# Optimization experiments

Hardware: AMD Instinct MI355X
Metric: run time of the kernel (lower is better)

## Reference

```python
import jax, jax.numpy as jnp
import numpy as np

C = 1.0          # Poincare ball curvature
EPS = 1e-7
MAX_TANH_ARG = 1.0 - 1e-5
K = 5            # topk neighbors (hardcoded in the module)


def _norm(x):
    return jnp.clip(jnp.linalg.norm(x, axis=-1, keepdims=True), EPS)


def expmap0(u):
    # exp map at origin: tanh(sqrt(c)||u||) * u / (sqrt(c)||u||)
    sc = jnp.sqrt(C)
    n = _norm(u)
    return jnp.tanh(sc * n) * u / (sc * n)


def logmap0(x):
    # log map at origin: artanh(sqrt(c)||x||) * x / (sqrt(c)||x||)
    sc = jnp.sqrt(C)
    n = _norm(x)
    arg = jnp.clip(sc * n, EPS, MAX_TANH_ARG)
    return jnp.arctanh(arg) * x / (sc * n)


def mobius_add(x, y):
    x2 = jnp.sum(x * x, axis=-1, keepdims=True)
    y2 = jnp.sum(y * y, axis=-1, keepdims=True)
    xy = jnp.sum(x * y, axis=-1, keepdims=True)
    num = (1.0 + 2.0 * C * xy + C * y2) * x + (1.0 - C * x2) * y
    den = 1.0 + 2.0 * C * xy + (C * C) * x2 * y2
    return num / (den + EPS)


def setup_inputs() -> dict:
    key = jax.random.key(0)
    k1, k2, k3, k4 = jax.random.split(key, 4)
    B, SEQ_DIM, HYP_DIM, N = 2048, 768, 128, 100000
    z_seq = jax.random.normal(k1, (B, SEQ_DIM), dtype=jnp.float32)
    # node embeddings must lie inside the unit ball; scale keeps norms ~0.57
    node_emb = 0.05 * jax.random.normal(k2, (N, HYP_DIM), dtype=jnp.float32)
    W = 0.02 * jax.random.normal(k3, (HYP_DIM, SEQ_DIM), dtype=jnp.float32)
    b = jnp.zeros((HYP_DIM,), dtype=jnp.float32)
    return {"z_seq": z_seq, "node_emb": node_emb, "W": W, "b": b}


def reference(z_seq, node_emb, W, b):
    # linear projection (dropout is identity in eval mode)
    z_proj = z_seq @ W.T + b                     # (B, D)
    z_hyp = expmap0(z_proj)                      # (B, D) in Poincare ball
    # no-grad nearest-node lookup in tangent space
    z_tan = logmap0(z_hyp)                       # (B, D)
    n_tan = logmap0(node_emb)                    # (N, D)
    # squared euclidean distances (monotone in cdist -> same topk indices)
    d2 = (jnp.sum(z_tan * z_tan, axis=-1, keepdims=True)
          - 2.0 * (z_tan @ n_tan.T)
          + jnp.sum(n_tan * n_tan, axis=-1)[None, :])  # (B, N)
    _, idx = jax.lax.top_k(-d2, K)               # (B, K) smallest distances
    near = jnp.mean(node_emb[idx], axis=1)       # (B, D) gather-mean
    z_fused = mobius_add(z_hyp, near)
    return (z_fused, z_hyp)
```

## Files before the change

kernel.cpp:

```cpp
#include <hip/hip_runtime.h>
#include <hip/hip_bf16.h>
#include <math.h>

#define EPSF 1e-7f
#define MAXT 0.99999f

typedef __attribute__((ext_vector_type(8))) short short8v;
typedef __attribute__((ext_vector_type(4))) float f32x4;

constexpr int Bb = 2048;
constexpr int Ss = 768;
constexpr int Dd = 128;
constexpr int Nn = 100000;
constexpr int Kk = 5;
constexpr int HALF = Bb * Dd;
constexpr int NT = 128;
constexpr int TILE_BYTES = NT * Dd * 2;
constexpr float SBIAS = 16.0f;

constexpr int NCH8 = 8;
constexpr int CH8 = Nn / NCH8;
constexpr int TIL8 = 98;
constexpr int PAD8 = TIL8 * NT;
constexpr int RQ = 64;

constexpr int NCH16 = 16;
constexpr int CH16 = Nn / NCH16;
constexpr int TIL16 = (CH16 + NT - 1) / NT;
constexpr int RT = 128;

static __device__ __forceinline__ ushort f2bf(float x) {
  __hip_bfloat16 h = __float2bfloat16(x);
  return *reinterpret_cast<ushort*>(&h);
}

static __device__ __forceinline__ float med3f(float a, float b, float c) {
  float r;
  asm("v_med3_f32 %0, %1, %2, %3" : "=v"(r) : "v"(a), "v"(b), "v"(c));
  return r;
}

static __device__ __forceinline__ void ins5f(float* k, float v) {
  const float n0 = fminf(k[0], v);
  const float n1 = med3f(k[0], k[1], v);
  const float n2 = med3f(k[1], k[2], v);
  const float n3 = med3f(k[2], k[3], v);
  const float n4 = med3f(k[3], k[4], v);
  k[0] = n0; k[1] = n1; k[2] = n2; k[3] = n3; k[4] = n4;
}

#define INS5(TV, TI, V, ID) do { \
  const float _v = (V); const int _id = (ID); \
  if (_v < TV[4]) { \
    TV[4] = _v; TI[4] = _id; \
    if (TV[4] < TV[3]) { float _t=TV[3];TV[3]=TV[4];TV[4]=_t;int _u=TI[3];TI[3]=TI[4];TI[4]=_u; } \
    if (TV[3] < TV[2]) { float _t=TV[2];TV[2]=TV[3];TV[3]=_t;int _u=TI[2];TI[2]=TI[3];TI[3]=_u; } \
    if (TV[2] < TV[1]) { float _t=TV[1];TV[1]=TV[2];TV[2]=_t;int _u=TI[1];TI[1]=TI[2];TI[2]=_u; } \
    if (TV[1] < TV[0]) { float _t=TV[0];TV[0]=TV[1];TV[1]=_t;int _u=TI[0];TI[0]=TI[1];TI[1]=_u; } \
  } } while(0)

#define LXLT(V,I,V2,I2) ((V) < (V2) || ((V) == (V2) && (I) < (I2)))
#define INS5L(TV, TI, V, ID) do { \
  const float _v = (V); const int _id = (ID); \
  if (LXLT(_v,_id,TV[4],TI[4])) { \
    TV[4]=_v; TI[4]=_id; \
    if (LXLT(TV[4],TI[4],TV[3],TI[3])) { float _t=TV[3];TV[3]=TV[4];TV[4]=_t;int _u=TI[3];TI[3]=TI[4];TI[4]=_u; } \
    if (LXLT(TV[3],TI[3],TV[2],TI[2])) { float _t=TV[2];TV[2]=TV[3];TV[3]=_t;int _u=TI[2];TI[2]=TI[3];TI[3]=_u; } \
    if (LXLT(TV[2],TI[2],TV[1],TI[1])) { float _t=TV[1];TV[1]=TV[2];TV[2]=_t;int _u=TI[1];TI[1]=TI[2];TI[2]=_u; } \
    if (LXLT(TV[1],TI[1],TV[0],TI[0])) { float _t=TV[0];TV[0]=TV[1];TV[1]=_t;int _u=TI[0];TI[0]=TI[1];TI[1]=_u; } \
  } } while(0)

static __device__ __forceinline__ void proj_body(
    const float* __restrict__ zseq, const float* __restrict__ W,
    const float* __restrict__ bias, float* __restrict__ outH,
    ushort* __restrict__ ztb, int blk,
    float (*zrow)[768], float (*zp)[128], float (*php)[128], float* rno)
{
  const int tid = threadIdx.x;
  const int d = tid & 127, h = tid >> 7;
  const int r0 = blk * 8;

  {
    const float4* src = reinterpret_cast<const float4*>(zseq + (size_t)r0 * Ss);
    float4* dst = reinterpret_cast<float4*>(&zrow[0][0]);
    #pragma unroll
    for (int i = 0; i < 6; ++i) dst[i * 256 + tid] = src[i * 256 + tid];
  }
  __syncthreads();

  float acc[8];
  #pragma unroll
  for (int r = 0; r < 8; ++r) acc[r] = 0.f;
  const float4* w4 = reinterpret_cast<const float4*>(W + (size_t)d * Ss) + h * 96;
  for (int j = 0; j < 96; ++j) {
    const float4 w = w4[j];
    const int kb = h * 384 + j * 4;
    #pragma unroll
    for (int r = 0; r < 8; ++r) {
      const float4 z = *reinterpret_cast<const float4*>(&zrow[r][kb]);
      acc[r] = fmaf(z.x, w.x, acc[r]);
      acc[r] = fmaf(z.y, w.y, acc[r]);
      acc[r] = fmaf(z.z, w.z, acc[r]);
      acc[r] = fmaf(z.w, w.w, acc[r]);
    }
  }
  #pragma unroll
  for (int r = 0; r < 8; ++r) {
    if (h == 0) zp[r][d] = acc[r]; else php[r][d] = acc[r];
  }
  __syncthreads();
  if (tid < 128) {
    const float bv = bias[d];
    #pragma unroll
    for (int r = 0; r < 8; ++r) zp[r][d] = zp[r][d] + php[r][d] + bv;
  }
  __syncthreads();

  const int wv = tid >> 6, ln = tid & 63;
  if (tid < 128) {
    #pragma unroll
    for (int rr = 0; rr < 4; ++rr) {
      const int r = wv * 4 + rr;
      float v = zp[r][ln] * zp[r][ln] + zp[r][ln + 64] * zp[r][ln + 64];
      #pragma unroll
      for (int off = 32; off > 0; off >>= 1) v += __shfl_xor(v, off);
      if (ln == 0) rno[r] = v;
    }
  }
  __syncthreads();
  if (tid < 128) {
    #pragma unroll
    for (int r = 0; r < 8; ++r) {
      const float n = fmaxf(sqrtf(rno[r]), EPSF);
      const float zh = tanhf(n) * zp[r][d] / n;
      outH[(size_t)(r0 + r) * Dd + d] = zh;
      zp[r][d] = zh;
    }
  }
  __syncthreads();
  if (tid < 128) {
    #pragma unroll
    for (int rr = 0; rr < 4; ++rr) {
      const int r = wv * 4 + rr;
      float v = zp[r][ln] * zp[r][ln] + zp[r][ln + 64] * zp[r][ln + 64];
      #pragma unroll
      for (int off = 32; off > 0; off >>= 1) v += __shfl_xor(v, off);
      if (ln == 0) rno[r] = v;
    }
  }
  __syncthreads();
  if (tid < 128) {
    #pragma unroll
    for (int r = 0; r < 8; ++r) {
      const float m = fmaxf(sqrtf(rno[r]), EPSF);
      const float a = atanhf(fminf(m, MAXT));
      ztb[(size_t)(r0 + r) * Dd + d] = f2bf(a * zp[r][d] / m);
    }
  }
}

__global__ __launch_bounds__(256) void k_proj(
    const float* __restrict__ zseq, const float* __restrict__ W,
    const float* __restrict__ bias, float* __restrict__ outH,
    ushort* __restrict__ ztb)
{
  __shared__ __align__(16) float zrow[8][768];
  __shared__ float zp[8][128];
  __shared__ float php[8][128];
  __shared__ float rno[8];
  proj_body(zseq, W, bias, outH, ztb, blockIdx.x, zrow, zp, php, rno);
}

__global__ __launch_bounds__(256) void k_prep(
    const float* __restrict__ zseq, const float* __restrict__ W,
    const float* __restrict__ bias, float* __restrict__ outH,
    ushort* __restrict__ ztb, const float* __restrict__ emb,
    ushort* __restrict__ embsw, float* __restrict__ cpad)
{
  __shared__ __align__(16) float zrow[8][768];
  __shared__ float zp[8][128];
  __shared__ float php[8][128];
  __shared__ float rno[8];

  if (blockIdx.x < Bb / 8) {
    proj_body(zseq, W, bias, outH, ztb, blockIdx.x, zrow, zp, php, rno);
    return;
  }

  const int wv = threadIdx.x >> 6, ln = threadIdx.x & 63;
  const int p = (blockIdx.x - Bb / 8) * 4 + wv;
  const int chunk = p / PAD8;
  const int local = p - chunk * PAD8;
  const bool real = local < CH8;
  const int node = chunk * CH8 + local;
  float2 v = make_float2(0.f, 0.f);
  if (real) v = *reinterpret_cast<const float2*>(emb + (size_t)node * Dd + ln * 2);
  float t = v.x * v.x + v.y * v.y;
  #pragma unroll
  for (int off = 32; off > 0; off >>= 1) t += __shfl_xor(t, off);

  const float E = fmaxf(sqrtf(t), EPSF);
  const float a = atanhf(fminf(E, MAXT));
  const float s = a / E;
  const float m2s = -2.f * s;

  const int tt = local >> 7, nd = local & 127;
  ushort2 w; w.x = f2bf(m2s * v.x); w.y = f2bf(m2s * v.y);
  char* dst = reinterpret_cast<char*>(embsw)
            + ((size_t)((chunk * TIL8 + tt) * NT + nd) << 8)
            + ((ln * 4) ^ ((nd & 7) << 4));
  *reinterpret_cast<ushort2*>(dst) = w;

  if (ln == 0) cpad[p] = real ? (s * s * t + SBIAS) : 3.0e38f;
}

__global__ __launch_bounds__(1024, 4) void k_topk8(
    const ushort* __restrict__ ztb, const ushort* __restrict__ embsw,
    const float* __restrict__ cpad, float* __restrict__ candV,
    int* __restrict__ candI)
{
  __shared__ __align__(16) ushort Bsm[2][NT * Dd];
  __shared__ __align__(16) float cb[2][NT];

  const int tid = threadIdx.x;
  const int ln = tid & 63;
  const int wv8 = (tid >> 6) & 7;
  const int qh = tid >> 9;
  const int ln15 = ln & 15;
  const int g = ln >> 4;
  const int chunk = blockIdx.x & 7;
  const int rowBase = (blockIdx.x >> 3) * RQ;
  const int qBase = rowBase + qh * 32;
  const char* embc = reinterpret_cast<const char*>(embsw)
                   + (size_t)chunk * (TIL8 * TILE_BYTES);
  const float* cch = cpad + (size_t)chunk * PAD8;

  short8v zfr[2][4];
  #pragma unroll
  for (int f = 0; f < 2; ++f)
    #pragma unroll
    for (int ks = 0; ks < 4; ++ks)
      zfr[f][ks] = *reinterpret_cast<const short8v*>(
          ztb + (size_t)(qBase + 16 * f + ln15) * Dd + 32 * ks + 8 * g);

  int rdoff[4];
  #pragma unroll
  for (int ks = 0; ks < 4; ++ks)
    rdoff[ks] = (wv8 * 16 + ln15) * 256 + ((ks * 64 + g * 16) ^ ((ln15 & 7) << 4));
  const int coff = wv8 * 64 + g * 16;
  const unsigned lanebase = (unsigned)(wv8 * 16 + 4 * g);

  float tv0[5], tv1[5];
  const float KINIT = __uint_as_float(0x7F7FFFFFu);
  #pragma unroll
  for (int q = 0; q < 5; ++q) { tv0[q] = KINIT; tv1[q] = KINIT; }

  const char* srcP = embc + tid * 16;
  const float* cbP = cch + tid;

  auto stage = [&](int buf) {
    char* lb = reinterpret_cast<char*>(&Bsm[buf][0]) + tid * 16;
    #pragma unroll
    for (int i = 0; i < 2; ++i) {
      __builtin_amdgcn_global_load_lds(
          (const __attribute__((address_space(1))) unsigned int*)(srcP + i * 16384),
          (__attribute__((address_space(3))) unsigned int*)(lb + i * 16384),
          16, 0, 0);
    }
    if (tid < NT) {
      __builtin_amdgcn_global_load_lds(
          (const __attribute__((address_space(1))) unsigned int*)cbP,
          (__attribute__((address_space(3))) unsigned int*)(&cb[buf][tid]),
          4, 0, 0);
    }
    srcP += TILE_BYTES;
    cbP += NT;
  };

  asm volatile("s_waitcnt vmcnt(0)" ::: "memory");
  stage(0);
  stage(1);

  for (int t = 0; t < TIL8; ++t) {
    const int buf = t & 1;
    if (t == TIL8 - 1) {
      asm volatile("s_waitcnt vmcnt(0)" ::: "memory");
    } else if (tid < 128) {
      asm volatile("s_waitcnt vmcnt(3)" ::: "memory");
    } else {
      asm volatile("s_waitcnt vmcnt(2)" ::: "memory");
    }
    __builtin_amdgcn_s_barrier();

    const char* bbase = reinterpret_cast<const char*>(&Bsm[buf][0]);
    short8v ae[4];
    #pragma unroll
    for (int ks = 0; ks < 4; ++ks)
      ae[ks] = *reinterpret_cast<const short8v*>(bbase + rdoff[ks]);
    const f32x4 cinit = *reinterpret_cast<const f32x4*>(
        reinterpret_cast<const char*>(&cb[buf][0]) + coff);

    __builtin_amdgcn_s_setprio(1);
    f32x4 a0 = __builtin_amdgcn_mfma_f32_16x16x32_bf16(ae[0], zfr[0][0], cinit, 0, 0, 0);
    f32x4 a1 = __builtin_amdgcn_mfma_f32_16x16x32_bf16(ae[0], zfr[1][0], cinit, 0, 0, 0);
    #pragma unroll
    for (int ks = 1; ks < 4; ++ks) {
      a0 = __builtin_amdgcn_mfma_f32_16x16x32_bf16(ae[ks], zfr[0][ks], a0, 0, 0, 0);
      a1 = __builtin_amdgcn_mfma_f32_16x16x32_bf16(ae[ks], zfr[1][ks], a1, 0, 0, 0);
    }
    __builtin_amdgcn_s_setprio(0);

    const unsigned ib = (unsigned)(t * NT) + lanebase;
    {
      const float k0 = __uint_as_float((__float_as_uint(a0[0]) & 0xFFFFC000u) | ib);
      const float k1 = __uint_as_float((__float_as_uint(a0[1]) & 0xFFFFC000u) | (ib + 1));
      const float k2 = __uint_as_float((__float_as_uint(a0[2]) & 0xFFFFC000u) | (ib + 2));
      const float k3 = __uint_as_float((__float_as_uint(a0[3]) & 0xFFFFC000u) | (ib + 3));
      ins5f(tv0, fminf(fminf(k0, k1), fminf(k2, k3)));
    }
    {
      const float k0 = __uint_as_float((__float_as_uint(a1[0]) & 0xFFFFC000u) | ib);
      const float k1 = __uint_as_float((__float_as_uint(a1[1]) & 0xFFFFC000u) | (ib + 1));
      const float k2 = __uint_as_float((__float_as_uint(a1[2]) & 0xFFFFC000u) | (ib + 2));
      const float k3 = __uint_as_float((__float_as_uint(a1[3]) & 0xFFFFC000u) | (ib + 3));
      ins5f(tv1, fminf(fminf(k0, k1), fminf(k2, k3)));
    }

    __builtin_amdgcn_s_barrier();
    asm volatile("" ::: "memory");
    if (t + 2 < TIL8) stage(buf);
  }

  #pragma unroll
  for (int m = 16; m <= 32; m <<= 1) {
    float ov[5];
    #pragma unroll
    for (int q = 0; q < 5; ++q) ov[q] = __shfl_xor(tv0[q], m);
    #pragma unroll
    for (int q = 0; q < 5; ++q) ins5f(tv0, ov[q]);
    #pragma unroll
    for (int q = 0; q < 5; ++q) ov[q] = __shfl_xor(tv1[q], m);
    #pragma unroll
    for (int q = 0; q < 5; ++q) ins5f(tv1, ov[q]);
  }
  __syncthreads();
  float* mgk = reinterpret_cast<float*>(&Bsm[0][0]);
  if (ln < 16) {
    #pragma unroll
    for (int q = 0; q < 5; ++q) {
      mgk[((qh * 32 + 0 + ln) * 8 + wv8) * Kk + q] = tv0[q];
      mgk[((qh * 32 + 16 + ln) * 8 + wv8) * Kk + q] = tv1[q];
    }
  }
  __syncthreads();
  if (tid < RQ) {
    float mv[5];
    #pragma unroll
    for (int q = 0; q < 5; ++q) mv[q] = mgk[(tid * 8 + 0) * Kk + q];
    for (int w = 1; w < 8; ++w)
      #pragma unroll
      for (int q = 0; q < 5; ++q) ins5f(mv, mgk[(tid * 8 + w) * Kk + q]);
    const size_t o = ((size_t)(rowBase + tid) * NCH8 + chunk) * Kk;
    #pragma unroll
    for (int q = 0; q < 5; ++q) {
      const unsigned u = __float_as_uint(mv[q]);
      candV[o + q] = __uint_as_float(u & 0xFFFFC000u);
      candI[o + q] = chunk * CH8 + (int)(u & 0x3FFFu);
    }
  }
}

__global__ __launch_bounds__(256) void k_node(
    const float* __restrict__ emb, float* __restrict__ sArr, float* __restrict__ cArr)
{
  const int wv = threadIdx.x >> 6, ln = threadIdx.x & 63;
  const int node = blockIdx.x * 4 + wv;
  const float2 v = *reinterpret_cast<const float2*>(emb + (size_t)node * Dd + ln * 2);
  float t = v.x * v.x + v.y * v.y;
  #pragma unroll
  for (int off = 32; off > 0; off >>= 1) t += __shfl_xor(t, off);
  if (ln == 0) {
    const float E = fmaxf(sqrtf(t), EPSF);
    const float a = atanhf(fminf(E, MAXT));
    const float s = a / E;
    sArr[node] = s;
    cArr[node] = s * s * t;
  }
}

__global__ __launch_bounds__(512, 2) void k_topk16(
    const ushort* __restrict__ ztb, const float* __restrict__ emb,
    const float* __restrict__ sArr, const float* __restrict__ cArr,
    float* __restrict__ candV, int* __restrict__ candI)
{
  __shared__ __align__(16) ushort Bsm[2][NT * Dd];
  __shared__ __align__(16) float2 sclb[2][NT];
  __shared__ __align__(16) float mgv[RT][2][Kk];
  __shared__ int mgi[RT][2][Kk];

  const int tid = threadIdx.x;
  const int ln = tid & 63;
  const int wv = tid >> 6;
  const int ln15 = ln & 15;
  const int g = ln >> 4;
  const int wr = wv >> 1;
  const int wc = wv & 1;
  const int rowBase = blockIdx.x * RT;
  const int chunkStart = blockIdx.y * CH16;

  short8v afr[2][4];
  #pragma unroll
  for (int f = 0; f < 2; ++f)
    #pragma unroll
    for (int ks = 0; ks < 4; ++ks)
      afr[f][ks] = *reinterpret_cast<const short8v*>(
          ztb + (size_t)(rowBase + 32 * wr + 16 * f + ln15) * Dd + 32 * ks + 8 * g);

  int rdoff[4];
  #pragma unroll
  for (int ks = 0; ks < 4; ++ks)
    rdoff[ks] = (wc * 64 + ln15) * 256 + ((g * 16 + ks * 64) ^ ((ln15 & 7) << 4));

  f32x4 acc[2][4];
  #pragma unroll
  for (int f = 0; f < 2; ++f)
    #pragma unroll
    for (int c = 0; c < 4; ++c) acc[f][c] = (f32x4)0.f;

  float tv[8][5]; int ti[8][5];
  #pragma unroll
  for (int r = 0; r < 8; ++r)
    #pragma unroll
    for (int q = 0; q < 5; ++q) { tv[r][q] = 3.0e38f; ti[r][q] = 0x7fffffff; }

  float4 ld[8];

  auto stageLoad = [&](int t) {
    const int tStart = t * NT;
    const int left = CH16 - tStart;
    #pragma unroll
    for (int i = 0; i < 8; ++i) {
      const int flat = i * 512 + tid;
      const int nd = flat >> 5;
      float4 v = make_float4(0.f, 0.f, 0.f, 0.f);
      if (nd < left)
        v = *reinterpret_cast<const float4*>(
            emb + (size_t)(chunkStart + tStart + nd) * Dd + (flat & 31) * 4);
      ld[i] = v;
    }
  };

  auto stageWrite = [&](int t, int buf) {
    char* base = reinterpret_cast<char*>(&Bsm[buf][0]);
    #pragma unroll
    for (int i = 0; i < 8; ++i) {
      const int flat = i * 512 + tid;
      const int nd = flat >> 5;
      const int kb = (flat & 31) * 8;
      ushort4 w;
      w.x = f2bf(ld[i].x); w.y = f2bf(ld[i].y);
      w.z = f2bf(ld[i].z); w.w = f2bf(ld[i].w);
      *reinterpret_cast<ushort4*>(base + nd * 256 + (kb ^ ((nd & 7) << 4))) = w;
    }
    const int tStart = t * NT;
    const int left = CH16 - tStart;
    if (tid < NT) {
      const bool ok = tid < left;
      sclb[buf][tid] = make_float2(ok ? -2.f * sArr[chunkStart + tStart + tid] : 0.f,
                                   ok ? cArr[chunkStart + tStart + tid] : 3.0e38f);
    }
  };

  stageLoad(0);
  stageWrite(0, 0);
  __syncthreads();

  for (int t = 0; t < TIL16; ++t) {
    const int buf = t & 1;
    const bool have = (t + 1) < TIL16;
    if (have) stageLoad(t + 1);

    const char* bbase = reinterpret_cast<const char*>(&Bsm[buf][0]);
    #pragma unroll
    for (int c = 0; c < 4; ++c) {
      #pragma unroll
      for (int ks = 0; ks < 4; ++ks) {
        const short8v bfr = *reinterpret_cast<const short8v*>(bbase + c * 4096 + rdoff[ks]);
        acc[0][c] = __builtin_amdgcn_mfma_f32_16x16x32_bf16(afr[0][ks], bfr, acc[0][c], 0, 0, 0);
        acc[1][c] = __builtin_amdgcn_mfma_f32_16x16x32_bf16(afr[1][ks], bfr, acc[1][c], 0, 0, 0);
      }
    }

    if (have) stageWrite(t + 1, buf ^ 1);

    #pragma unroll
    for (int c = 0; c < 4; ++c) {
      const int nl = wc * 64 + c * 16 + ln15;
      const float2 sc2 = sclb[buf][nl];
      const int node = chunkStart + t * NT + nl;
      #pragma unroll
      for (int f = 0; f < 2; ++f) {
        #pragma unroll
        for (int i = 0; i < 4; ++i) {
          const float v = fmaf(sc2.x, acc[f][c][i], sc2.y);
          INS5(tv[f * 4 + i], ti[f * 4 + i], v, node);
        }
        acc[f][c] = (f32x4)0.f;
      }
    }
    __syncthreads();
  }

  #pragma unroll
  for (int m = 1; m <= 8; m <<= 1) {
    #pragma unroll
    for (int r = 0; r < 8; ++r) {
      float ov[5]; int oi[5];
      #pragma unroll
      for (int q = 0; q < 5; ++q) {
        ov[q] = __shfl_xor(tv[r][q], m);
        oi[q] = __shfl_xor(ti[r][q], m);
      }
      #pragma unroll
      for (int q = 0; q < 5; ++q) INS5L(tv[r], ti[r], ov[q], oi[q]);
    }
  }
  if (ln15 == 0) {
    #pragma unroll
    for (int f = 0; f < 2; ++f)
      #pragma unroll
      for (int i = 0; i < 4; ++i) {
        const int row = 32 * wr + 16 * f + 4 * g + i;
        #pragma unroll
        for (int q = 0; q < 5; ++q) {
          mgv[row][wc][q] = tv[f * 4 + i][q];
          mgi[row][wc][q] = ti[f * 4 + i][q];
        }
      }
  }
  __syncthreads();
  if (tid < RT) {
    float mv[5]; int mi[5];
    #pragma unroll
    for (int q = 0; q < 5; ++q) { mv[q] = mgv[tid][0][q]; mi[q] = mgi[tid][0][q]; }
    #pragma unroll
    for (int q = 0; q < 5; ++q) INS5L(mv, mi, mgv[tid][1][q], mgi[tid][1][q]);
    const size_t o = ((size_t)(rowBase + tid) * NCH16 + blockIdx.y) * Kk;
    #pragma unroll
    for (int q = 0; q < 5; ++q) { candV[o + q] = mv[q]; candI[o + q] = mi[q]; }
  }
}

__global__ __launch_bounds__(256) void k_fuse(
    const float* __restrict__ emb, const float* __restrict__ candV,
    const int* __restrict__ candI, const float* __restrict__ zhyp,
    float* __restrict__ out, int ncand)
{
  const int wv = threadIdx.x >> 6, ln = threadIdx.x & 63;
  const int row = blockIdx.x * 4 + wv;

  float mv[5]; int mi[5];
  #pragma unroll
  for (int q = 0; q < 5; ++q) { mv[q] = 3.0e38f; mi[q] = 0x7fffffff; }
  const size_t base = (size_t)row * ncand;
  for (int j = ln; j < ncand; j += 64) INS5L(mv, mi, candV[base + j], candI[base + j]);
  #pragma unroll
  for (int m = 1; m <= 32; m <<= 1) {
    float ov[5]; int oi[5];
    #pragma unroll
    for (int q = 0; q < 5; ++q) { ov[q] = __shfl_xor(mv[q], m); oi[q] = __shfl_xor(mi[q], m); }
    #pragma unroll
    for (int q = 0; q < 5; ++q) INS5L(mv, mi, ov[q], oi[q]);
  }
  float y0 = 0.f, y1 = 0.f;
  #pragma unroll
  for (int q = 0; q < Kk; ++q) {
    const float* e = emb + (size_t)mi[q] * Dd;
    y0 += e[ln]; y1 += e[ln + 64];
  }
  y0 *= 0.2f; y1 *= 0.2f;
  const float x0 = zhyp[(size_t)row * Dd + ln];
  const float x1 = zhyp[(size_t)row * Dd + ln + 64];
  float x2 = x0 * x0 + x1 * x1;
  float y2 = y0 * y0 + y1 * y1;
  float xy = x0 * y0 + x1 * y1;
  #pragma unroll
  for (int off = 32; off > 0; off >>= 1) {
    x2 += __shfl_xor(x2, off);
    y2 += __shfl_xor(y2, off);
    xy += __shfl_xor(xy, off);
  }
  const float ca = 1.f + 2.f * xy + y2;
  const float cb2 = 1.f - x2;
  const float den = 1.f / (1.f + 2.f * xy + x2 * y2 + EPSF);
  out[(size_t)row * Dd + ln] = (ca * x0 + cb2 * y0) * den;
  out[(size_t)row * Dd + ln + 64] = (ca * x1 + cb2 * y1) * den;
}

extern "C" void kernel_launch(void* const* d_in, const int* in_sizes, int n_in,
                              void* d_out, int out_size, void* d_ws, size_t ws_size,
                              hipStream_t stream)
{
  (void)in_sizes; (void)n_in; (void)out_size;
  const float* zseq = (const float*)d_in[0];
  const float* emb  = (const float*)d_in[1];
  const float* W    = (const float*)d_in[2];
  const float* bias = (const float*)d_in[3];
  float* out = (float*)d_out;

  const size_t ztbBytes   = (size_t)Bb * Dd * 2;
  const size_t embswBytes = (size_t)NCH8 * TIL8 * TILE_BYTES;
  const size_t cpadBytes  = (size_t)NCH8 * PAD8 * 4;
  const size_t candVBytes = (size_t)Bb * NCH8 * Kk * 4;
  const size_t needFast = ztbBytes + embswBytes + cpadBytes + 2 * candVBytes;

  if (ws_size >= needFast) {
    char* ws = (char*)d_ws;
    ushort* ztb   = (ushort*)ws;
    ushort* embsw = (ushort*)(ws + ztbBytes);
    float*  cpad  = (float*)(ws + ztbBytes + embswBytes);
    float*  candV = (float*)(ws + ztbBytes + embswBytes + cpadBytes);
    int*    candI = (int*)(ws + ztbBytes + embswBytes + cpadBytes + candVBytes);

    hipLaunchKernelGGL(k_prep, dim3(Bb / 8 + NCH8 * PAD8 / 4), dim3(256), 0,
                       stream, zseq, W, bias, out + HALF, ztb, emb, embsw, cpad);
    hipLaunchKernelGGL(k_topk8, dim3(256), dim3(1024), 0, stream,
                       ztb, embsw, cpad, candV, candI);
    hipLaunchKernelGGL(k_fuse, dim3(Bb / 4), dim3(256), 0, stream,
                       emb, candV, candI, out + HALF, out, NCH8 * Kk);
  } else {
    char* ws = (char*)d_ws;
    ushort* ztb  = (ushort*)ws;
    float* sArr  = (float*)(ws + ztbBytes);
    float* cArr  = sArr + Nn;
    float* candV = cArr + Nn;
    int*   candI = (int*)(candV + (size_t)Bb * NCH16 * Kk);

    hipLaunchKernelGGL(k_proj, dim3(Bb / 8), dim3(256), 0, stream,
                       zseq, W, bias, out + HALF, ztb);
    hipLaunchKernelGGL(k_node, dim3(Nn / 4), dim3(256), 0, stream, emb, sArr, cArr);
    hipLaunchKernelGGL(k_topk16, dim3(Bb / RT, NCH16), dim3(512), 0, stream,
                       ztb, emb, sArr, cArr, candV, candI);
    hipLaunchKernelGGL(k_fuse, dim3(Bb / 4), dim3(256), 0, stream,
                       emb, candV, candI, out + HALF, out, NCH16 * Kk);
  }
}
```

Before: 144.9 us.

## Process two tiles per barrier stage and merge their minima before top-k insert

The top-k scan kernel now stages super-tiles of two 128-node tiles per double-buffer slot. Each slot is consumed with one barrier pair instead of two, and the per-lane minima of both tiles are combined before a single top-5 insertion. This halves barrier and insertion overhead per tile. The cost is double the LDS footprint, to about 128 KB, which likely caps residency at one 1024-thread block per CU. Keeping one minimum per eight candidates instead of per four may also drop true neighbours from the per-lane candidate list.

After: 131.9 us. 1.1x faster.

```diff
diff --git a/kernel.cpp b/kernel.cpp
--- a/kernel.cpp
+++ b/kernel.cpp
@@ -16,11 +16,13 @@
 constexpr int HALF = Bb * Dd;
 constexpr int NT = 128;
 constexpr int TILE_BYTES = NT * Dd * 2;
+constexpr int SUP_BYTES = 2 * TILE_BYTES;
 constexpr float SBIAS = 16.0f;
 
 constexpr int NCH8 = 8;
 constexpr int CH8 = Nn / NCH8;
 constexpr int TIL8 = 98;
+constexpr int NSUP = TIL8 / 2;
 constexpr int PAD8 = TIL8 * NT;
 constexpr int RQ = 64;
 
@@ -219,8 +221,8 @@
     const float* __restrict__ cpad, float* __restrict__ candV,
     int* __restrict__ candI)
 {
-  __shared__ __align__(16) ushort Bsm[2][NT * Dd];
-  __shared__ __align__(16) float cb[2][NT];
+  __shared__ __align__(16) ushort Bsm[2][2][NT * Dd];
+  __shared__ __align__(16) float cb[2][2 * NT];
 
   const int tid = threadIdx.x;
   const int ln = tid & 63;
@@ -259,76 +261,82 @@
   const float* cbP = cch + tid;
 
   auto stage = [&](int buf) {
-    char* lb = reinterpret_cast<char*>(&Bsm[buf][0]) + tid * 16;
-    #pragma unroll
-    for (int i = 0; i < 2; ++i) {
+    char* lb = reinterpret_cast<char*>(&Bsm[buf][0][0]) + tid * 16;
+    #pragma unroll
+    for (int i = 0; i < 4; ++i) {
       __builtin_amdgcn_global_load_lds(
           (const __attribute__((address_space(1))) unsigned int*)(srcP + i * 16384),
           (__attribute__((address_space(3))) unsigned int*)(lb + i * 16384),
           16, 0, 0);
     }
-    if (tid < NT) {
+    if (tid < 2 * NT) {
       __builtin_amdgcn_global_load_lds(
           (const __attribute__((address_space(1))) unsigned int*)cbP,
           (__attribute__((address_space(3))) unsigned int*)(&cb[buf][tid]),
           4, 0, 0);
     }
-    srcP += TILE_BYTES;
-    cbP += NT;
+    srcP += SUP_BYTES;
+    cbP += 2 * NT;
   };
 
   asm volatile("s_waitcnt vmcnt(0)" ::: "memory");
   stage(0);
   stage(1);
 
-  for (int t = 0; t < TIL8; ++t) {
-    const int buf = t & 1;
-    if (t == TIL8 - 1) {
+  for (int st = 0; st < NSUP; ++st) {
+    const int buf = st & 1;
+    if (st == NSUP - 1) {
       asm volatile("s_waitcnt vmcnt(0)" ::: "memory");
-    } else if (tid < 128) {
-      asm volatile("s_waitcnt vmcnt(3)" ::: "memory");
+    } else if (tid < 2 * NT) {
+      asm volatile("s_waitcnt vmcnt(5)" ::: "memory");
     } else {
-      asm volatile("s_waitcnt vmcnt(2)" ::: "memory");
+      asm volatile("s_waitcnt vmcnt(4)" ::: "memory");
     }
     __builtin_amdgcn_s_barrier();
 
-    const char* bbase = reinterpret_cast<const char*>(&Bsm[buf][0]);
-    short8v ae[4];
-    #pragma unroll
-    for (int ks = 0; ks < 4; ++ks)
-      ae[ks] = *reinterpret_cast<const short8v*>(bbase + rdoff[ks]);
-    const f32x4 cinit = *reinterpret_cast<const f32x4*>(
-        reinterpret_cast<const char*>(&cb[buf][0]) + coff);
-
-    __builtin_amdgcn_s_setprio(1);
-    f32x4 a0 = __builtin_amdgcn_mfma_f32_16x16x32_bf16(ae[0], zfr[0][0], cinit, 0, 0, 0);
-    f32x4 a1 = __builtin_amdgcn_mfma_f32_16x16x32_bf16(ae[0], zfr[1][0], cinit, 0, 0, 0);
-    #pragma unroll
-    for (int ks = 1; ks < 4; ++ks) {
-      a0 = __builtin_amdgcn_mfma_f32_16x16x32_bf16(ae[ks], zfr[0][ks], a0, 0, 0, 0);
-      a1 = __builtin_amdgcn_mfma_f32_16x16x32_bf16(ae[ks], zfr[1][ks], a1, 0, 0, 0);
-    }
-    __builtin_amdgcn_s_setprio(0);
-
-    const unsigned ib = (unsigned)(t * NT) + lanebase;
-    {
-      const float k0 = __uint_as_float((__float_as_uint(a0[0]) & 0xFFFFC000u) | ib);
-      const float k1 = __uint_as_float((__float_as_uint(a0[1]) & 0xFFFFC000u) | (ib + 1));
-      const float k2 = __uint_as_float((__float_as_uint(a0[2]) & 0xFFFFC000u) | (ib + 2));
-      const float k3 = __uint_as_float((__float_as_uint(a0[3]) & 0xFFFFC000u) | (ib + 3));
-      ins5f(tv0, fminf(fminf(k0, k1), fminf(k2, k3)));
-    }
-    {
-      const float k0 = __uint_as_float((__float_as_uint(a1[0]) & 0xFFFFC000u) | ib);
-      const float k1 = __uint_as_float((__float_as_uint(a1[1]) & 0xFFFFC000u) | (ib + 1));
-      const float k2 = __uint_as_float((__float_as_uint(a1[2]) & 0xFFFFC000u) | (ib + 2));
-      const float k3 = __uint_as_float((__float_as_uint(a1[3]) & 0xFFFFC000u) | (ib + 3));
-      ins5f(tv1, fminf(fminf(k0, k1), fminf(k2, k3)));
-    }
+    float mm0 = KINIT, mm1 = KINIT;
+    #pragma unroll
+    for (int u = 0; u < 2; ++u) {
+      const char* bbase = reinterpret_cast<const char*>(&Bsm[buf][u][0]);
+      short8v ae[4];
+      #pragma unroll
+      for (int ks = 0; ks < 4; ++ks)
+        ae[ks] = *reinterpret_cast<const short8v*>(bbase + rdoff[ks]);
+      const f32x4 cinit = *reinterpret_cast<const f32x4*>(
+          reinterpret_cast<const char*>(&cb[buf][u * NT]) + coff);
+
+      __builtin_amdgcn_s_setprio(1);
+      f32x4 a0 = __builtin_amdgcn_mfma_f32_16x16x32_bf16(ae[0], zfr[0][0], cinit, 0, 0, 0);
+      f32x4 a1 = __builtin_amdgcn_mfma_f32_16x16x32_bf16(ae[0], zfr[1][0], cinit, 0, 0, 0);
+      #pragma unroll
+      for (int ks = 1; ks < 4; ++ks) {
+        a0 = __builtin_amdgcn_mfma_f32_16x16x32_bf16(ae[ks], zfr[0][ks], a0, 0, 0, 0);
+        a1 = __builtin_amdgcn_mfma_f32_16x16x32_bf16(ae[ks], zfr[1][ks], a1, 0, 0, 0);
+      }
+      __builtin_amdgcn_s_setprio(0);
+
+      const unsigned ib = (unsigned)((2 * st + u) * NT) + lanebase;
+      {
+        const float k0 = __uint_as_float((__float_as_uint(a0[0]) & 0xFFFFC000u) | ib);
+        const float k1 = __uint_as_float((__float_as_uint(a0[1]) & 0xFFFFC000u) | (ib + 1));
+        const float k2 = __uint_as_float((__float_as_uint(a0[2]) & 0xFFFFC000u) | (ib + 2));
+        const float k3 = __uint_as_float((__float_as_uint(a0[3]) & 0xFFFFC000u) | (ib + 3));
+        mm0 = fminf(mm0, fminf(fminf(k0, k1), fminf(k2, k3)));
+      }
+      {
+        const float k0 = __uint_as_float((__float_as_uint(a1[0]) & 0xFFFFC000u) | ib);
+        const float k1 = __uint_as_float((__float_as_uint(a1[1]) & 0xFFFFC000u) | (ib + 1));
+        const float k2 = __uint_as_float((__float_as_uint(a1[2]) & 0xFFFFC000u) | (ib + 2));
+        const float k3 = __uint_as_float((__float_as_uint(a1[3]) & 0xFFFFC000u) | (ib + 3));
+        mm1 = fminf(mm1, fminf(fminf(k0, k1), fminf(k2, k3)));
+      }
+    }
+    ins5f(tv0, mm0);
+    ins5f(tv1, mm1);
 
     __builtin_amdgcn_s_barrier();
     asm volatile("" ::: "memory");
-    if (t + 2 < TIL8) stage(buf);
+    if (st + 2 < NSUP) stage(buf);
   }
 
   #pragma unroll
@@ -344,7 +352,7 @@
     for (int q = 0; q < 5; ++q) ins5f(tv1, ov[q]);
   }
   __syncthreads();
-  float* mgk = reinterpret_cast<float*>(&Bsm[0][0]);
+  float* mgk = reinterpret_cast<float*>(&Bsm[0][0][0]);
   if (ln < 16) {
     #pragma unroll
     for (int q = 0; q < 5; ++q) {
```
